# Optimization experiments

Measured on AMD Instinct MI355X. Metric: run time of the kernel, lower is better.

Reference implementation:

```python
import jax, jax.numpy as jnp
import numpy as np

B, S, W, D, A = 64, 512, 256, 768, 32


def setup_inputs() -> dict:
    key = jax.random.key(0)
    k1, k2, k3 = jax.random.split(key, 3)
    sequence_output = jax.random.normal(k1, (B, S, D), dtype=jnp.float32)
    # head-subword indices per example (valid, sorted, in [0, S))
    word_idxs = jnp.sort(jax.random.randint(k2, (B, W), 0, S), axis=-1)
    cls_w = jax.random.normal(k3, (A, 3, D), dtype=jnp.float32) * 0.02
    cls_b = jnp.zeros((A, 3), dtype=jnp.float32)
    return {"sequence_output": sequence_output, "word_idxs": word_idxs,
            "cls_w": cls_w, "cls_b": cls_b}


def reference(sequence_output, word_idxs, cls_w, cls_b):
    # Original builds a [B, W, S] one-hot pooler matrix and does bmm with
    # sequence_output [B, S, D]; since rows are one-hot at word head positions,
    # this is exactly a gather along the subword axis.
    pooled = jnp.take_along_axis(sequence_output, word_idxs[..., None], axis=1)  # [B, W, D]
    # dropout is identity at inference. Fused per-attribute Linear(768, 3):
    logits = jnp.einsum("bwd,acd->abwc", pooled, cls_w) + cls_b[:, None, None, :]  # [A, B, W, 3]
    return logits
```

## Files before the change

### kernel.cpp

```cpp
#include <hip/hip_runtime.h>
#include <hip/hip_bf16.h>

#define B_    64
#define S_    512
#define W_    256
#define D_    768
#define NN    96
#define BK    64
#define NCH   12

typedef __attribute__((ext_vector_type(8))) short bfrag;
typedef __attribute__((ext_vector_type(4))) float f32x4;
typedef __attribute__((ext_vector_type(4))) short s16x4;

static __device__ __forceinline__ short f2bf(float f) {
  __hip_bfloat16 h = __float2bfloat16(f);
  return __builtin_bit_cast(short, h);
}
static __device__ __forceinline__ s16x4 pack4(f32x4 v) {
  s16x4 r;
  r[0] = f2bf(v[0]); r[1] = f2bf(v[1]); r[2] = f2bf(v[2]); r[3] = f2bf(v[3]);
  return r;
}

__global__ __launch_bounds__(768, 6) void ner_kernel(
    const float* __restrict__ seq, const int* __restrict__ widx,
    const float* __restrict__ cw, const float* __restrict__ cb,
    float* __restrict__ out)
{
  __shared__ union {
    struct {
      short a[32 * 64];
      short b[96 * 64];
    } s;
    float o[32 * 100];
  } u;

  const int tid = threadIdx.x;
  const int blk = blockIdx.x;
  const int b   = blk >> 3;
  const int w0  = (blk & 7) << 5;

  const int srow = tid >> 4;
  const int kc   = tid & 15;
  const float* aptr = nullptr;
  if (tid < 512) {
    const int sidx = widx[b * W_ + w0 + srow];
    aptr = seq + ((size_t)b * S_ + sidx) * D_ + kc * 4;
  }
  const int brow1 = srow + 48;
  const float* bptr0 = cw + (size_t)srow  * D_ + kc * 4;
  const float* bptr1 = cw + (size_t)brow1 * D_ + kc * 4;

  const int lane = tid & 63;
  const int wv   = tid >> 6;
  const int mt   = wv & 1;
  const int nt   = wv >> 1;
  const int r16  = lane & 15;
  const int g    = lane >> 4;

  const int am = mt * 16 + r16;
  const int bn = nt * 16 + r16;

  f32x4 acc = {0.f, 0.f, 0.f, 0.f};

  char* const la = (char*)u.s.a;
  char* const lb = (char*)u.s.b;

  f32x4 ra, rb0, rb1;
  if (tid < 512) ra = *(const f32x4*)(aptr);
  rb0 = *(const f32x4*)(bptr0);
  rb1 = *(const f32x4*)(bptr1);

  for (int c = 0; c < NCH; ++c) {
    __syncthreads();
    if (tid < 512)
      *(s16x4*)(la + srow  * 128 + ((kc * 8) ^ ((srow  & 7) << 4))) = pack4(ra);
    *(s16x4*)(lb + srow  * 128 + ((kc * 8) ^ ((srow  & 7) << 4))) = pack4(rb0);
    *(s16x4*)(lb + brow1 * 128 + ((kc * 8) ^ ((brow1 & 7) << 4))) = pack4(rb1);
    __syncthreads();
    if (c + 1 < NCH) {
      const int k0 = (c + 1) * BK;
      if (tid < 512) ra = *(const f32x4*)(aptr + k0);
      rb0 = *(const f32x4*)(bptr0 + k0);
      rb1 = *(const f32x4*)(bptr1 + k0);
    }
    #pragma unroll
    for (int ks = 0; ks < 2; ++ks) {
      bfrag af = *(const bfrag*)(la + am * 128 + (((ks * 64) + g * 16) ^ ((am & 7) << 4)));
      bfrag bf = *(const bfrag*)(lb + bn * 128 + (((ks * 64) + g * 16) ^ ((bn & 7) << 4)));
      acc = __builtin_amdgcn_mfma_f32_16x16x32_bf16(af, bf, acc, 0, 0, 0);
    }
  }

  __syncthreads();
  {
    const int n    = nt * 16 + r16;
    const float bias = cb[n];
    const int row0 = mt * 16 + g * 4;
    #pragma unroll
    for (int j = 0; j < 4; ++j)
      u.o[(row0 + j) * 100 + n] = acc[j] + bias;
  }
  __syncthreads();
  {
    const int a  = tid / 24;
    const int e0 = (tid % 24) * 4;
    float vv[4];
    #pragma unroll
    for (int q = 0; q < 4; ++q) {
      const int e = e0 + q;
      vv[q] = u.o[(e / 3) * 100 + a * 3 + (e - (e / 3) * 3)];
    }
    float* op = out + ((size_t)(a * B_ + b) * W_ + w0) * 3 + e0;
    *(float4*)op = make_float4(vv[0], vv[1], vv[2], vv[3]);
  }
}

extern "C" void kernel_launch(void* const* d_in, const int* in_sizes, int n_in,
                              void* d_out, int out_size, void* d_ws, size_t ws_size,
                              hipStream_t stream) {
  const float* seq  = (const float*)d_in[0];
  const int*   widx = (const int*)d_in[1];
  const float* cw   = (const float*)d_in[2];
  const float* cb   = (const float*)d_in[3];
  float* out = (float*)d_out;

  dim3 grid(B_ * (W_ / 32));
  dim3 block(768);
  ner_kernel<<<grid, block, 0, stream>>>(seq, widx, cw, cb, out);
}
```

Before: 143.5 us.

## Pre-pack weights to bf16 MFMA fragments and load full gathered rows once

```diff
diff --git a/kernel.cpp b/kernel.cpp
--- a/kernel.cpp
+++ b/kernel.cpp
@@ -6,8 +6,6 @@
 #define W_    256
 #define D_    768
 #define NN    96
-#define BK    64
-#define NCH   12
 
 typedef __attribute__((ext_vector_type(8))) short bfrag;
 typedef __attribute__((ext_vector_type(4))) float f32x4;
@@ -23,16 +21,29 @@
   return r;
 }
 
+__global__ void pack_b_kernel(const float* __restrict__ cw, short* __restrict__ pb) {
+  const int t    = blockIdx.x * 256 + threadIdx.x;
+  const int lane = t & 63;
+  const int tile = t >> 6;
+  const int kk   = tile % 24;
+  const int nt   = tile / 24;
+  const int n    = nt * 16 + (lane & 15);
+  const int k    = kk * 32 + (lane >> 4) * 8;
+  const float* src = cw + (size_t)n * D_ + k;
+  f32x4 lo = *(const f32x4*)src;
+  f32x4 hi = *(const f32x4*)(src + 4);
+  s16x4* dst = (s16x4*)(pb + (size_t)t * 8);
+  dst[0] = pack4(lo);
+  dst[1] = pack4(hi);
+}
+
 __global__ __launch_bounds__(768, 6) void ner_kernel(
     const float* __restrict__ seq, const int* __restrict__ widx,
-    const float* __restrict__ cw, const float* __restrict__ cb,
+    const short* __restrict__ pb, const float* __restrict__ cb,
     float* __restrict__ out)
 {
   __shared__ union {
-    struct {
-      short a[32 * 64];
-      short b[96 * 64];
-    } s;
+    short a[32 * D_];
     float o[32 * 100];
   } u;
 
@@ -41,16 +52,25 @@
   const int b   = blk >> 3;
   const int w0  = (blk & 7) << 5;
 
-  const int srow = tid >> 4;
-  const int kc   = tid & 15;
-  const float* aptr = nullptr;
-  if (tid < 512) {
-    const int sidx = widx[b * W_ + w0 + srow];
-    aptr = seq + ((size_t)b * S_ + sidx) * D_ + kc * 4;
+  const int col4  = tid % 192;
+  const int rbase = tid / 192;
+  const float* rowp[8];
+  #pragma unroll
+  for (int p = 0; p < 8; ++p) {
+    const int r    = p * 4 + rbase;
+    const int sidx = widx[b * W_ + w0 + r];
+    rowp[p] = seq + ((size_t)b * S_ + sidx) * D_ + col4 * 4;
   }
-  const int brow1 = srow + 48;
-  const float* bptr0 = cw + (size_t)srow  * D_ + kc * 4;
-  const float* bptr1 = cw + (size_t)brow1 * D_ + kc * 4;
+  f32x4 va[8];
+  #pragma unroll
+  for (int p = 0; p < 8; ++p) va[p] = *(const f32x4*)rowp[p];
+  char* const la = (char*)u.a;
+  #pragma unroll
+  for (int p = 0; p < 8; ++p) {
+    const int r = p * 4 + rbase;
+    *(s16x4*)(la + r * 1536 + ((col4 * 8) ^ ((r & 7) << 4))) = pack4(va[p]);
+  }
+  __syncthreads();
 
   const int lane = tid & 63;
   const int wv   = tid >> 6;
@@ -58,46 +78,25 @@
   const int nt   = wv >> 1;
   const int r16  = lane & 15;
   const int g    = lane >> 4;
+  const int am   = mt * 16 + r16;
 
-  const int am = mt * 16 + r16;
-  const int bn = nt * 16 + r16;
+  const short* bp = pb + ((size_t)(nt * 24) * 64 + lane) * 8;
 
-  f32x4 acc = {0.f, 0.f, 0.f, 0.f};
-
-  char* const la = (char*)u.s.a;
-  char* const lb = (char*)u.s.b;
-
-  f32x4 ra, rb0, rb1;
-  if (tid < 512) ra = *(const f32x4*)(aptr);
-  rb0 = *(const f32x4*)(bptr0);
-  rb1 = *(const f32x4*)(bptr1);
-
-  for (int c = 0; c < NCH; ++c) {
-    __syncthreads();
-    if (tid < 512)
-      *(s16x4*)(la + srow  * 128 + ((kc * 8) ^ ((srow  & 7) << 4))) = pack4(ra);
-    *(s16x4*)(lb + srow  * 128 + ((kc * 8) ^ ((srow  & 7) << 4))) = pack4(rb0);
-    *(s16x4*)(lb + brow1 * 128 + ((kc * 8) ^ ((brow1 & 7) << 4))) = pack4(rb1);
-    __syncthreads();
-    if (c + 1 < NCH) {
-      const int k0 = (c + 1) * BK;
-      if (tid < 512) ra = *(const f32x4*)(aptr + k0);
-      rb0 = *(const f32x4*)(bptr0 + k0);
-      rb1 = *(const f32x4*)(bptr1 + k0);
-    }
-    #pragma unroll
-    for (int ks = 0; ks < 2; ++ks) {
-      bfrag af = *(const bfrag*)(la + am * 128 + (((ks * 64) + g * 16) ^ ((am & 7) << 4)));
-      bfrag bf = *(const bfrag*)(lb + bn * 128 + (((ks * 64) + g * 16) ^ ((bn & 7) << 4)));
-      acc = __builtin_amdgcn_mfma_f32_16x16x32_bf16(af, bf, acc, 0, 0, 0);
-    }
+  f32x4 acc0 = {0.f,0.f,0.f,0.f}, acc1 = {0.f,0.f,0.f,0.f};
+  #pragma unroll 4
+  for (int kk = 0; kk < 24; ++kk) {
+    bfrag af = *(const bfrag*)(la + am * 1536 + ((kk * 64 + g * 16) ^ ((am & 7) << 4)));
+    bfrag bf = *(const bfrag*)(bp + (size_t)kk * 512);
+    if (kk & 1) acc1 = __builtin_amdgcn_mfma_f32_16x16x32_bf16(af, bf, acc1, 0, 0, 0);
+    else        acc0 = __builtin_amdgcn_mfma_f32_16x16x32_bf16(af, bf, acc0, 0, 0, 0);
   }
+  const f32x4 acc = acc0 + acc1;
 
   __syncthreads();
   {
-    const int n    = nt * 16 + r16;
+    const int n     = nt * 16 + r16;
     const float bias = cb[n];
-    const int row0 = mt * 16 + g * 4;
+    const int row0  = mt * 16 + g * 4;
     #pragma unroll
     for (int j = 0; j < 4; ++j)
       u.o[(row0 + j) * 100 + n] = acc[j] + bias;
@@ -124,9 +123,9 @@
   const int*   widx = (const int*)d_in[1];
   const float* cw   = (const float*)d_in[2];
   const float* cb   = (const float*)d_in[3];
-  float* out = (float*)d_out;
+  float* out  = (float*)d_out;
+  short* pb   = (short*)d_ws;
 
-  dim3 grid(B_ * (W_ / 32));
-  dim3 block(768);
-  ner_kernel<<<grid, block, 0, stream>>>(seq, widx, cw, cb, out);
+  pack_b_kernel<<<36, 256, 0, stream>>>(cw, pb);
+  ner_kernel<<<B_ * (W_ / 32), 768, 0, stream>>>(seq, widx, pb, cb, out);
 }
```

Result: no change. 145.4 us (+1.3%).
